# Performance work log

Hardware: AMD Instinct MI355X
Metric: run time of the kernel (lower is better)

Reference implementation:

```python
import jax, jax.numpy as jnp
import numpy as np

C_HID = 128   # c = int(c2 * e) = 128
N_EXP = 4
TOP_K = 2


def conv2d(x, w, b, padding='SAME'):
    # x: [B,Cin,H,W], w: [Cout,Cin,kh,kw]
    out = jax.lax.conv_general_dilated(
        x, w, window_strides=(1, 1), padding=padding,
        dimension_numbers=('NCHW', 'OIHW', 'NCHW'))
    return out + b[None, :, None, None]


def silu(x):
    return x * jax.nn.sigmoid(x)


def setup_inputs() -> dict:
    key = jax.random.key(0)
    ks = jax.random.split(key, 10)
    B, C1, H, W = 16, 256, 80, 80
    c = C_HID
    s = 0.05
    return {
        'x': jax.random.normal(ks[0], (B, C1, H, W), jnp.float32),
        'W_cv1': jax.random.normal(ks[1], (2 * c, C1, 1, 1), jnp.float32) * s,
        'b_cv1': jax.random.normal(ks[2], (2 * c,), jnp.float32) * s,
        'W_r': jax.random.normal(ks[3], (N_EXP, c), jnp.float32) * s,
        'b_r': jax.random.normal(ks[4], (N_EXP,), jnp.float32) * s,
        'W_exp': jax.random.normal(ks[5], (N_EXP, c, c, 3, 3), jnp.float32) * s,
        'b_exp': jax.random.normal(ks[6], (N_EXP, c), jnp.float32) * s,
        'W_cv2': jax.random.normal(ks[7], (256, 3 * c, 1, 1), jnp.float32) * s,
        'b_cv2': jax.random.normal(ks[8], (256,), jnp.float32) * s,
    }


def reference(x, W_cv1, b_cv1, W_r, b_r, W_exp, b_exp, W_cv2, b_cv2):
    c = C_HID
    B = x.shape[0]
    # cv1: 1x1 conv -> SiLU (BN folded into bias), split into two branches
    y = silu(conv2d(x, W_cv1, b_cv1))           # [B, 2c, H, W]
    a, m = y[:, :c], y[:, c:]                   # each [B, c, H, W]

    # CrossModalRouter: GAP -> linear -> softmax -> top-k -> renormalize
    pooled = m.mean(axis=(2, 3))                # [B, c]
    logits = pooled @ W_r.T + b_r               # [B, E]
    probs = jax.nn.softmax(logits, axis=-1)
    w, idx = jax.lax.top_k(probs, TOP_K)        # [B, k]
    w = w / w.sum(axis=-1, keepdims=True)

    # dense sparse-gate: zeros except the top-k entries
    gate = jnp.zeros((B, N_EXP), x.dtype).at[jnp.arange(B)[:, None], idx].set(w)

    # DualModalExpertContainer: E independent 3x3 conv+SiLU experts, gated sum
    exp_out = jax.vmap(lambda we, be: silu(conv2d(m, we, be)))(W_exp, b_exp)  # [E,B,c,H,W]
    moe = jnp.einsum('be,ebchw->bchw', gate, exp_out)  # [B, c, H, W]

    # cv2 over concat([y0, y1, expert_out])
    out = silu(conv2d(jnp.concatenate([a, m, moe], axis=1), W_cv2, b_cv2))
    return out
```

## Files before the change

kernel.cpp:

```cpp
#include <hip/hip_runtime.h>
#include <hip/hip_bf16.h>

#define NPIX 6400
#define IMW 80
#define IMH 80

typedef __attribute__((ext_vector_type(8))) short short8;
typedef __attribute__((ext_vector_type(4))) float floatx4;

__device__ __forceinline__ float silu_f(float v) {
    return v / (1.0f + __expf(-v));
}
__device__ __forceinline__ unsigned short f2bf(float v) {
    __hip_bfloat16 h = __float2bfloat16(v);
    return *(unsigned short*)&h;
}


__global__ __launch_bounds__(256) void prep_swz1(
    const float* __restrict__ W1, __hip_bfloat16* __restrict__ Wt1s)
{
    int t = blockIdx.x * 256 + threadIdx.x;
    int mt = t >> 9, rem = t & 511;
    int ks = rem >> 6, lane = rem & 63;
    int col = lane & 15, quad = lane >> 4;
    const float* src = W1 + (size_t)(mt * 16 + col) * 256 + ks * 32 + quad * 8;
    unsigned short pk[8];
    #pragma unroll
    for (int j = 0; j < 8; ++j) pk[j] = f2bf(src[j]);
    *(uint4*)(Wt1s + (size_t)t * 8) = *(uint4*)pk;
}

__global__ __launch_bounds__(256) void prep_swz2(
    const float* __restrict__ W2, __hip_bfloat16* __restrict__ Wt2s)
{
    int t = blockIdx.x * 256 + threadIdx.x;
    int mt = t / 768, rem = t % 768;
    int ks = rem >> 6, lane = rem & 63;
    int col = lane & 15, quad = lane >> 4;
    const float* src = W2 + (size_t)(mt * 16 + col) * 384 + ks * 32 + quad * 8;
    unsigned short pk[8];
    #pragma unroll
    for (int j = 0; j < 8; ++j) pk[j] = f2bf(src[j]);
    *(uint4*)(Wt2s + (size_t)t * 8) = *(uint4*)pk;
}

__global__ __launch_bounds__(256) void prep_swzE(
    const float* __restrict__ Wexp, __hip_bfloat16* __restrict__ Wts)
{
    int t = blockIdx.x * 256 + threadIdx.x;
    int e = t / 18432, rem = t % 18432;
    int gmt = rem / 2304, rem2 = rem % 2304;
    int s = rem2 >> 6, lane = rem2 & 63;
    int col = lane & 15, quad = lane >> 4;
    int tap = s >> 2;
    int cib = (s & 3) * 32 + quad * 8;
    int co  = gmt * 16 + col;
    const float* src = Wexp + ((size_t)(e * 128 + co) * 128 + cib) * 9 + tap;
    unsigned short pk[8];
    #pragma unroll
    for (int j = 0; j < 8; ++j) pk[j] = f2bf(src[j * 9]);
    *(uint4*)(Wts + (size_t)t * 8) = *(uint4*)pk;
}

__global__ __launch_bounds__(256, 2) void cv1_fused(
    const float* __restrict__ x, const __hip_bfloat16* __restrict__ Wt1s,
    const float* __restrict__ b1, __hip_bfloat16* __restrict__ catT,
    float* __restrict__ pooled)
{
    __shared__ __align__(16) unsigned short xs[128][256];
    const int b  = blockIdx.y;
    const int p0 = blockIdx.x * 128;
    const int tid = threadIdx.x;

    {
        const int ci = tid;
        const int slotbase = (ci >> 3) ;
        const int cilo = ci & 7;
        const float* src = x + ((size_t)b * 256 + ci) * NPIX + p0;
        #pragma unroll
        for (int pg = 0; pg < 32; ++pg) {
            float4 v = *(const float4*)(src + pg * 4);
            float vv[4] = {v.x, v.y, v.z, v.w};
            #pragma unroll
            for (int r = 0; r < 4; ++r) {
                int pix = pg * 4 + r;
                int slot = slotbase ^ ((pix & 7) << 2);
                xs[pix][slot * 8 + cilo] = f2bf(vv[r]);
            }
        }
    }
    __syncthreads();

    const int wave = tid >> 6, lane = tid & 63;
    const int col = lane & 15, quad = lane >> 4;
    const int cohalf  = (wave & 1) * 128;
    const int gmt0    = (wave & 1) * 8;
    const int pixhalf = (wave >> 1) * 64;

    __hip_bfloat16* ct = catT + (size_t)b * NPIX * 384;
    int pp[4], pl[4];
    #pragma unroll
    for (int nt = 0; nt < 4; ++nt) {
        pl[nt] = pixhalf + nt * 16 + col;
        pp[nt] = p0 + pl[nt];
    }

    floatx4 acc[8][4] = {};

    #pragma unroll
    for (int ks = 0; ks < 8; ++ks) {
        short8 bf[4];
        #pragma unroll
        for (int nt = 0; nt < 4; ++nt) {
            int slot = (ks * 4 + quad) ^ ((pl[nt] & 7) << 2);
            bf[nt] = *(const short8*)&xs[pl[nt]][slot * 8];
        }
        #pragma unroll
        for (int mt = 0; mt < 8; ++mt) {
            short8 af = *(const short8*)&Wt1s[(size_t)(((gmt0 + mt) * 8 + ks) * 64 + lane) * 8];
            #pragma unroll
            for (int nt = 0; nt < 4; ++nt)
                acc[mt][nt] = __builtin_amdgcn_mfma_f32_16x16x32_bf16(af, bf[nt], acc[mt][nt], 0, 0, 0);
        }
    }

    #pragma unroll
    for (int mt = 0; mt < 8; ++mt) {
        const int cobase = cohalf + mt * 16 + quad * 4;
        float bias[4];
        #pragma unroll
        for (int r = 0; r < 4; ++r) bias[r] = b1[cobase + r];
        float v[4][4];
        #pragma unroll
        for (int nt = 0; nt < 4; ++nt) {
            unsigned short pk[4];
            #pragma unroll
            for (int r = 0; r < 4; ++r) {
                v[nt][r] = silu_f(acc[mt][nt][r] + bias[r]);
                pk[r] = f2bf(v[nt][r]);
            }
            *(uint2*)&ct[(size_t)pp[nt] * 384 + cobase] = *(uint2*)pk;
        }
        if (cohalf == 128) {
            #pragma unroll
            for (int r = 0; r < 4; ++r) {
                float s = v[0][r] + v[1][r] + v[2][r] + v[3][r];
                #pragma unroll
                for (int m = 1; m < 16; m <<= 1)
                    s += __shfl_xor(s, m, 64);
                if (col == 0)
                    atomicAdd(&pooled[b * 128 + (cobase - 128) + r], s * (1.0f / NPIX));
            }
        }
    }
}

__global__ __launch_bounds__(64) void router_kernel(
    const float* __restrict__ pooled, const float* __restrict__ Wr,
    const float* __restrict__ br, int* __restrict__ sel_idx, float* __restrict__ sel_w)
{
    __shared__ float lg[16][4];
    int tid = threadIdx.x;
    int b = tid >> 2, e = tid & 3;
    float s = br[e];
    for (int c2 = 0; c2 < 128; c2++)
        s += pooled[b * 128 + c2] * Wr[e * 128 + c2];
    lg[b][e] = s;
    __syncthreads();
    if (tid < 16) {
        int bb = tid;
        float l[4]; float mx = -1e30f;
        #pragma unroll
        for (int i = 0; i < 4; i++) { l[i] = lg[bb][i]; mx = fmaxf(mx, l[i]); }
        float p[4]; float sum = 0.f;
        #pragma unroll
        for (int i = 0; i < 4; i++) { p[i] = __expf(l[i] - mx); sum += p[i]; }
        #pragma unroll
        for (int i = 0; i < 4; i++) p[i] /= sum;
        int i1 = 0;
        for (int i = 1; i < 4; i++) if (p[i] > p[i1]) i1 = i;
        int i2 = (i1 == 0) ? 1 : 0;
        for (int i = 0; i < 4; i++) if (i != i1 && p[i] > p[i2]) i2 = i;
        float inv = 1.0f / (p[i1] + p[i2]);
        sel_idx[bb * 2 + 0] = i1; sel_idx[bb * 2 + 1] = i2;
        sel_w[bb * 2 + 0] = p[i1] * inv; sel_w[bb * 2 + 1] = p[i2] * inv;
    }
}

__global__ __launch_bounds__(256, 2) void expert_gemm(
    __hip_bfloat16* __restrict__ catT, const __hip_bfloat16* __restrict__ Wts,
    const float* __restrict__ bexp, const int* __restrict__ sel_idx,
    const float* __restrict__ sel_w)
{
    __shared__ __align__(16) __hip_bfloat16 wl[64 * 512];

    const int id  = blockIdx.x;
    const int xcd = id & 7, j = id >> 3;
    const int lin = xcd * 100 + j;
    const int b   = lin / 50;
    const int p0  = (lin % 50) * 128;

    const int e0 = sel_idx[b * 2 + 0], e1 = sel_idx[b * 2 + 1];
    const float g0 = sel_w[b * 2 + 0], g1 = sel_w[b * 2 + 1];

    const int tid  = threadIdx.x;
    const int wave = tid >> 6, lane = tid & 63;
    const int col  = lane & 15, quad = lane >> 4;
    const int cohalf  = (wave & 1) * 64;
    const int gmt0    = (wave & 1) * 4;
    const int pixhalf = (wave >> 1) * 64;

    __hip_bfloat16* ct = catT + (size_t)b * NPIX * 384;
    const __hip_bfloat16* wbase[2];
    wbase[0] = Wts + (size_t)e0 * (8 * 36 * 64 * 8);
    wbase[1] = Wts + (size_t)e1 * (8 * 36 * 64 * 8);

    int pp[4], prow[4], pcol[4];
    #pragma unroll
    for (int nt = 0; nt < 4; ++nt) {
        pp[nt]   = p0 + pixhalf + nt * 16 + col;
        prow[nt] = pp[nt] / IMW;
        pcol[nt] = pp[nt] % IMW;
    }

    floatx4 acc[2][4][4] = {};

    for (int tap = 0; tap < 9; ++tap) {
        const int dyy = tap / 3 - 1, dxx = tap % 3 - 1;

        __syncthreads();
        #pragma unroll
        for (int i = 0; i < 16; ++i) {
            int c   = wave * 16 + i;
            int ce  = c >> 5;
            int rem = c & 31;
            int gmt = rem >> 2, ss3 = rem & 3;
            const __hip_bfloat16* srcp = wbase[ce]
                + (size_t)((gmt * 36 + tap * 4 + ss3) * 64 + lane) * 8;
            __hip_bfloat16* dstp = &wl[c * 512];
            __builtin_amdgcn_global_load_lds(
                (const __attribute__((address_space(1))) unsigned int*)srcp,
                (__attribute__((address_space(3))) unsigned int*)dstp, 16, 0, 0);
        }
        __syncthreads();

        bool valid[4];
        const __hip_bfloat16* bbase[4];
        #pragma unroll
        for (int nt = 0; nt < 4; ++nt) {
            int ir = prow[nt] + dyy, ic = pcol[nt] + dxx;
            valid[nt] = ((unsigned)ir < IMH) && ((unsigned)ic < IMW);
            bbase[nt] = ct + (size_t)(ir * IMW + ic) * 384 + 128 + quad * 8;
        }
        #pragma unroll
        for (int ss = 0; ss < 4; ++ss) {
            short8 bf[4];
            #pragma unroll
            for (int nt = 0; nt < 4; ++nt) {
                int4 vv = {0, 0, 0, 0};
                if (valid[nt]) vv = *(const int4*)(bbase[nt] + ss * 32);
                bf[nt] = *(short8*)&vv;
            }
            __builtin_amdgcn_s_setprio(1);
            #pragma unroll
            for (int e = 0; e < 2; ++e) {
                #pragma unroll
                for (int mt = 0; mt < 4; ++mt) {
                    short8 af = *(const short8*)&wl[(size_t)((e * 8 + gmt0 + mt) * 4 + ss) * 512
                                                    + lane * 8];
                    #pragma unroll
                    for (int nt = 0; nt < 4; ++nt)
                        acc[e][mt][nt] = __builtin_amdgcn_mfma_f32_16x16x32_bf16(
                            af, bf[nt], acc[e][mt][nt], 0, 0, 0);
                }
            }
            __builtin_amdgcn_s_setprio(0);
        }
    }

    #pragma unroll
    for (int mt = 0; mt < 4; ++mt) {
        const int cobase = cohalf + mt * 16 + quad * 4;
        #pragma unroll
        for (int nt = 0; nt < 4; ++nt) {
            unsigned short pk[4];
            #pragma unroll
            for (int r = 0; r < 4; ++r) {
                int coo = cobase + r;
                float vb0 = bexp[e0 * 128 + coo];
                float vb1 = bexp[e1 * 128 + coo];
                float v = g0 * silu_f(acc[0][mt][nt][r] + vb0)
                        + g1 * silu_f(acc[1][mt][nt][r] + vb1);
                pk[r] = f2bf(v);
            }
            *(uint2*)&ct[(size_t)pp[nt] * 384 + 256 + cobase] = *(uint2*)pk;
        }
    }
}

__global__ __launch_bounds__(256, 2) void cv2_mfma(
    const __hip_bfloat16* __restrict__ catT, const __hip_bfloat16* __restrict__ Wt2s,
    const float* __restrict__ b2, float* __restrict__ out)
{
    const int b  = blockIdx.y;
    const int p0 = blockIdx.x * 128;
    const int tid = threadIdx.x;
    const int wave = tid >> 6, lane = tid & 63;
    const int col = lane & 15, quad = lane >> 4;
    const int cohalf  = (wave & 1) * 128;
    const int gmt0    = (wave & 1) * 8;
    const int pixhalf = (wave >> 1) * 64;

    const __hip_bfloat16* ct = catT + (size_t)b * NPIX * 384;
    int pp[4];
    #pragma unroll
    for (int nt = 0; nt < 4; ++nt) pp[nt] = p0 + pixhalf + nt * 16 + col;

    floatx4 acc[8][4] = {};

    #pragma unroll
    for (int ks = 0; ks < 12; ++ks) {
        short8 bf[4];
        #pragma unroll
        for (int nt = 0; nt < 4; ++nt)
            bf[nt] = *(const short8*)&ct[(size_t)pp[nt] * 384 + ks * 32 + quad * 8];
        #pragma unroll
        for (int mt = 0; mt < 8; ++mt) {
            short8 af = *(const short8*)&Wt2s[(size_t)(((gmt0 + mt) * 12 + ks) * 64 + lane) * 8];
            #pragma unroll
            for (int nt = 0; nt < 4; ++nt)
                acc[mt][nt] = __builtin_amdgcn_mfma_f32_16x16x32_bf16(af, bf[nt], acc[mt][nt], 0, 0, 0);
        }
    }

    #pragma unroll
    for (int mt = 0; mt < 8; ++mt) {
        const int cobase = cohalf + mt * 16 + quad * 4;
        #pragma unroll
        for (int r = 0; r < 4; ++r) {
            float bias = b2[cobase + r];
            size_t rowb = ((size_t)b * 256 + cobase + r) * NPIX;
            #pragma unroll
            for (int nt = 0; nt < 4; ++nt)
                out[rowb + pp[nt]] = silu_f(acc[mt][nt][r] + bias);
        }
    }
}

extern "C" void kernel_launch(void* const* d_in, const int* in_sizes, int n_in,
                              void* d_out, int out_size, void* d_ws, size_t ws_size,
                              hipStream_t stream)
{
    (void)in_sizes; (void)n_in; (void)out_size; (void)ws_size;
    const float* x    = (const float*)d_in[0];
    const float* W1   = (const float*)d_in[1];
    const float* b1   = (const float*)d_in[2];
    const float* Wr   = (const float*)d_in[3];
    const float* br   = (const float*)d_in[4];
    const float* Wexp = (const float*)d_in[5];
    const float* bexp = (const float*)d_in[6];
    const float* W2   = (const float*)d_in[7];
    const float* b2   = (const float*)d_in[8];
    float* out = (float*)d_out;

    char* ws = (char*)d_ws;
    __hip_bfloat16* catT = (__hip_bfloat16*)ws;
    __hip_bfloat16* Wts  = (__hip_bfloat16*)(ws + 78643200);
    __hip_bfloat16* Wt1s = (__hip_bfloat16*)(ws + 79822848);
    __hip_bfloat16* Wt2s = (__hip_bfloat16*)(ws + 79953920);
    float* pooled        = (float*)(ws + 80150528);
    int*   sel_idx       = (int*)(ws + 80158720);
    float* sel_w         = (float*)(ws + 80158848);

    hipMemsetAsync(pooled, 0, 16 * 128 * 4, stream);
    prep_swz1    <<<dim3(32),         256, 0, stream>>>(W1, Wt1s);
    prep_swz2    <<<dim3(48),         256, 0, stream>>>(W2, Wt2s);
    prep_swzE    <<<dim3(288),        256, 0, stream>>>(Wexp, Wts);
    cv1_fused    <<<dim3(50, 16),     256, 0, stream>>>(x, Wt1s, b1, catT, pooled);
    router_kernel<<<1,                 64, 0, stream>>>(pooled, Wr, br, sel_idx, sel_w);
    expert_gemm  <<<dim3(800),        256, 0, stream>>>(catT, Wts, bexp, sel_idx, sel_w);
    cv2_mfma     <<<dim3(50, 16),     256, 0, stream>>>(catT, Wt2s, b2, out);
}
```

Measured before the change: 422.7 us.

## Fuse expert conv and cv2 GEMM, keeping the MoE tile in LDS

Merges the expert 3x3 conv kernel and the cv2 1x1 conv kernel into one kernel. The gated MoE output for each 128-pixel tile is written into a swizzled LDS buffer instead of back to the catT workspace in global memory, and the cv2 GEMM reads its last 128 input channels from LDS. This removes the global store and reload of the MoE slice and one kernel launch. In exchange the fused kernel holds two accumulator sets in sequence, which may raise register pressure and lower occupancy.

```diff
diff --git a/kernel.cpp b/kernel.cpp
--- a/kernel.cpp
+++ b/kernel.cpp
@@ -188,10 +188,11 @@
     }
 }
 
-__global__ __launch_bounds__(256, 2) void expert_gemm(
-    __hip_bfloat16* __restrict__ catT, const __hip_bfloat16* __restrict__ Wts,
+__global__ __launch_bounds__(256, 2) void expert_cv2(
+    const __hip_bfloat16* __restrict__ catT, const __hip_bfloat16* __restrict__ Wts,
     const float* __restrict__ bexp, const int* __restrict__ sel_idx,
-    const float* __restrict__ sel_w)
+    const float* __restrict__ sel_w, const __hip_bfloat16* __restrict__ Wt2s,
+    const float* __restrict__ b2, float* __restrict__ out)
 {
     __shared__ __align__(16) __hip_bfloat16 wl[64 * 512];
 
@@ -211,7 +212,7 @@
     const int gmt0    = (wave & 1) * 4;
     const int pixhalf = (wave >> 1) * 64;
 
-    __hip_bfloat16* ct = catT + (size_t)b * NPIX * 384;
+    const __hip_bfloat16* ct = catT + (size_t)b * NPIX * 384;
     const __hip_bfloat16* wbase[2];
     wbase[0] = Wts + (size_t)e0 * (8 * 36 * 64 * 8);
     wbase[1] = Wts + (size_t)e1 * (8 * 36 * 64 * 8);
@@ -224,126 +225,128 @@
         pcol[nt] = pp[nt] % IMW;
     }
 
-    floatx4 acc[2][4][4] = {};
-
-    for (int tap = 0; tap < 9; ++tap) {
-        const int dyy = tap / 3 - 1, dxx = tap % 3 - 1;
+    {
+        floatx4 acc[2][4][4] = {};
+
+        for (int tap = 0; tap < 9; ++tap) {
+            const int dyy = tap / 3 - 1, dxx = tap % 3 - 1;
+
+            __syncthreads();
+            #pragma unroll
+            for (int i = 0; i < 16; ++i) {
+                int c   = wave * 16 + i;
+                int ce  = c >> 5;
+                int rem = c & 31;
+                int gmt = rem >> 2, ss3 = rem & 3;
+                const __hip_bfloat16* srcp = wbase[ce]
+                    + (size_t)((gmt * 36 + tap * 4 + ss3) * 64 + lane) * 8;
+                __hip_bfloat16* dstp = &wl[c * 512];
+                __builtin_amdgcn_global_load_lds(
+                    (const __attribute__((address_space(1))) unsigned int*)srcp,
+                    (__attribute__((address_space(3))) unsigned int*)dstp, 16, 0, 0);
+            }
+            __syncthreads();
+
+            bool valid[4];
+            const __hip_bfloat16* bbase[4];
+            #pragma unroll
+            for (int nt = 0; nt < 4; ++nt) {
+                int ir = prow[nt] + dyy, ic = pcol[nt] + dxx;
+                valid[nt] = ((unsigned)ir < IMH) && ((unsigned)ic < IMW);
+                bbase[nt] = ct + (size_t)(ir * IMW + ic) * 384 + 128 + quad * 8;
+            }
+            #pragma unroll
+            for (int ss = 0; ss < 4; ++ss) {
+                short8 bf[4];
+                #pragma unroll
+                for (int nt = 0; nt < 4; ++nt) {
+                    int4 vv = {0, 0, 0, 0};
+                    if (valid[nt]) vv = *(const int4*)(bbase[nt] + ss * 32);
+                    bf[nt] = *(short8*)&vv;
+                }
+                __builtin_amdgcn_s_setprio(1);
+                #pragma unroll
+                for (int e = 0; e < 2; ++e) {
+                    #pragma unroll
+                    for (int mt = 0; mt < 4; ++mt) {
+                        short8 af = *(const short8*)&wl[(size_t)((e * 8 + gmt0 + mt) * 4 + ss) * 512
+                                                        + lane * 8];
+                        #pragma unroll
+                        for (int nt = 0; nt < 4; ++nt)
+                            acc[e][mt][nt] = __builtin_amdgcn_mfma_f32_16x16x32_bf16(
+                                af, bf[nt], acc[e][mt][nt], 0, 0, 0);
+                    }
+                }
+                __builtin_amdgcn_s_setprio(0);
+            }
+        }
 
         __syncthreads();
         #pragma unroll
-        for (int i = 0; i < 16; ++i) {
-            int c   = wave * 16 + i;
-            int ce  = c >> 5;
-            int rem = c & 31;
-            int gmt = rem >> 2, ss3 = rem & 3;
-            const __hip_bfloat16* srcp = wbase[ce]
-                + (size_t)((gmt * 36 + tap * 4 + ss3) * 64 + lane) * 8;
-            __hip_bfloat16* dstp = &wl[c * 512];
-            __builtin_amdgcn_global_load_lds(
-                (const __attribute__((address_space(1))) unsigned int*)srcp,
-                (__attribute__((address_space(3))) unsigned int*)dstp, 16, 0, 0);
+        for (int mt = 0; mt < 4; ++mt) {
+            const int cobase = cohalf + mt * 16 + quad * 4;
+            const int slot16 = cobase >> 3;
+            const int off    = cobase & 7;
+            #pragma unroll
+            for (int nt = 0; nt < 4; ++nt) {
+                const int pixL = pixhalf + nt * 16 + col;
+                unsigned short pk[4];
+                #pragma unroll
+                for (int r = 0; r < 4; ++r) {
+                    int coo = cobase + r;
+                    float vb0 = bexp[e0 * 128 + coo];
+                    float vb1 = bexp[e1 * 128 + coo];
+                    float v = g0 * silu_f(acc[0][mt][nt][r] + vb0)
+                            + g1 * silu_f(acc[1][mt][nt][r] + vb1);
+                    pk[r] = f2bf(v);
+                }
+                *(uint2*)&wl[(size_t)pixL * 128 + ((slot16 ^ (pixL & 7)) * 8) + off] = *(uint2*)pk;
+            }
         }
         __syncthreads();
-
-        bool valid[4];
-        const __hip_bfloat16* bbase[4];
-        #pragma unroll
-        for (int nt = 0; nt < 4; ++nt) {
-            int ir = prow[nt] + dyy, ic = pcol[nt] + dxx;
-            valid[nt] = ((unsigned)ir < IMH) && ((unsigned)ic < IMW);
-            bbase[nt] = ct + (size_t)(ir * IMW + ic) * 384 + 128 + quad * 8;
-        }
-        #pragma unroll
-        for (int ss = 0; ss < 4; ++ss) {
+    }
+
+    {
+        const int cohalf2 = (wave & 1) * 128;
+        const int gmt0_2  = (wave & 1) * 8;
+
+        floatx4 acc2[8][4] = {};
+
+        #pragma unroll
+        for (int ks = 0; ks < 12; ++ks) {
             short8 bf[4];
-            #pragma unroll
-            for (int nt = 0; nt < 4; ++nt) {
-                int4 vv = {0, 0, 0, 0};
-                if (valid[nt]) vv = *(const int4*)(bbase[nt] + ss * 32);
-                bf[nt] = *(short8*)&vv;
-            }
-            __builtin_amdgcn_s_setprio(1);
-            #pragma unroll
-            for (int e = 0; e < 2; ++e) {
-                #pragma unroll
-                for (int mt = 0; mt < 4; ++mt) {
-                    short8 af = *(const short8*)&wl[(size_t)((e * 8 + gmt0 + mt) * 4 + ss) * 512
-                                                    + lane * 8];
-                    #pragma unroll
-                    for (int nt = 0; nt < 4; ++nt)
-                        acc[e][mt][nt] = __builtin_amdgcn_mfma_f32_16x16x32_bf16(
-                            af, bf[nt], acc[e][mt][nt], 0, 0, 0);
+            if (ks < 8) {
+                #pragma unroll
+                for (int nt = 0; nt < 4; ++nt)
+                    bf[nt] = *(const short8*)&ct[(size_t)pp[nt] * 384 + ks * 32 + quad * 8];
+            } else {
+                #pragma unroll
+                for (int nt = 0; nt < 4; ++nt) {
+                    const int pl = pixhalf + nt * 16 + col;
+                    const int s0 = (ks - 8) * 4 + quad;
+                    bf[nt] = *(const short8*)&wl[(size_t)pl * 128 + ((s0 ^ (pl & 7)) * 8)];
                 }
             }
-            __builtin_amdgcn_s_setprio(0);
-        }
-    }
-
-    #pragma unroll
-    for (int mt = 0; mt < 4; ++mt) {
-        const int cobase = cohalf + mt * 16 + quad * 4;
-        #pragma unroll
-        for (int nt = 0; nt < 4; ++nt) {
-            unsigned short pk[4];
+            #pragma unroll
+            for (int mt = 0; mt < 8; ++mt) {
+                short8 af = *(const short8*)&Wt2s[(size_t)(((gmt0_2 + mt) * 12 + ks) * 64 + lane) * 8];
+                #pragma unroll
+                for (int nt = 0; nt < 4; ++nt)
+                    acc2[mt][nt] = __builtin_amdgcn_mfma_f32_16x16x32_bf16(af, bf[nt], acc2[mt][nt], 0, 0, 0);
+            }
+        }
+
+        #pragma unroll
+        for (int mt = 0; mt < 8; ++mt) {
+            const int cobase = cohalf2 + mt * 16 + quad * 4;
             #pragma unroll
             for (int r = 0; r < 4; ++r) {
-                int coo = cobase + r;
-                float vb0 = bexp[e0 * 128 + coo];
-                float vb1 = bexp[e1 * 128 + coo];
-                float v = g0 * silu_f(acc[0][mt][nt][r] + vb0)
-                        + g1 * silu_f(acc[1][mt][nt][r] + vb1);
-                pk[r] = f2bf(v);
-            }
-            *(uint2*)&ct[(size_t)pp[nt] * 384 + 256 + cobase] = *(uint2*)pk;
-        }
-    }
-}
-
-__global__ __launch_bounds__(256, 2) void cv2_mfma(
-    const __hip_bfloat16* __restrict__ catT, const __hip_bfloat16* __restrict__ Wt2s,
-    const float* __restrict__ b2, float* __restrict__ out)
-{
-    const int b  = blockIdx.y;
-    const int p0 = blockIdx.x * 128;
-    const int tid = threadIdx.x;
-    const int wave = tid >> 6, lane = tid & 63;
-    const int col = lane & 15, quad = lane >> 4;
-    const int cohalf  = (wave & 1) * 128;
-    const int gmt0    = (wave & 1) * 8;
-    const int pixhalf = (wave >> 1) * 64;
-
-    const __hip_bfloat16* ct = catT + (size_t)b * NPIX * 384;
-    int pp[4];
-    #pragma unroll
-    for (int nt = 0; nt < 4; ++nt) pp[nt] = p0 + pixhalf + nt * 16 + col;
-
-    floatx4 acc[8][4] = {};
-
-    #pragma unroll
-    for (int ks = 0; ks < 12; ++ks) {
-        short8 bf[4];
-        #pragma unroll
-        for (int nt = 0; nt < 4; ++nt)
-            bf[nt] = *(const short8*)&ct[(size_t)pp[nt] * 384 + ks * 32 + quad * 8];
-        #pragma unroll
-        for (int mt = 0; mt < 8; ++mt) {
-            short8 af = *(const short8*)&Wt2s[(size_t)(((gmt0 + mt) * 12 + ks) * 64 + lane) * 8];
-            #pragma unroll
-            for (int nt = 0; nt < 4; ++nt)
-                acc[mt][nt] = __builtin_amdgcn_mfma_f32_16x16x32_bf16(af, bf[nt], acc[mt][nt], 0, 0, 0);
-        }
-    }
-
-    #pragma unroll
-    for (int mt = 0; mt < 8; ++mt) {
-        const int cobase = cohalf + mt * 16 + quad * 4;
-        #pragma unroll
-        for (int r = 0; r < 4; ++r) {
-            float bias = b2[cobase + r];
-            size_t rowb = ((size_t)b * 256 + cobase + r) * NPIX;
-            #pragma unroll
-            for (int nt = 0; nt < 4; ++nt)
-                out[rowb + pp[nt]] = silu_f(acc[mt][nt][r] + bias);
+                float bias = b2[cobase + r];
+                size_t rowb = ((size_t)b * 256 + cobase + r) * NPIX;
+                #pragma unroll
+                for (int nt = 0; nt < 4; ++nt)
+                    out[rowb + pp[nt]] = silu_f(acc2[mt][nt][r] + bias);
+            }
         }
     }
 }
@@ -379,6 +382,6 @@
     prep_swzE    <<<dim3(288),        256, 0, stream>>>(Wexp, Wts);
     cv1_fused    <<<dim3(50, 16),     256, 0, stream>>>(x, Wt1s, b1, catT, pooled);
     router_kernel<<<1,                 64, 0, stream>>>(pooled, Wr, br, sel_idx, sel_w);
-    expert_gemm  <<<dim3(800),        256, 0, stream>>>(catT, Wts, bexp, sel_idx, sel_w);
-    cv2_mfma     <<<dim3(50, 16),     256, 0, stream>>>(catT, Wt2s, b2, out);
-}
+    expert_cv2   <<<dim3(800),        256, 0, stream>>>(catT, Wts, bexp, sel_idx, sel_w,
+                                                        Wt2s, b2, out);
+}
```

Result: no change. 428.1 us (+1.3%).
